# Kernel optimization log

Measured on AMD Instinct MI355X. Metric: run time of the kernel, lower is better.

The kernel has to match this reference:

```python
import jax, jax.numpy as jnp
import numpy as np

NHEAD = 8

def setup_inputs() -> dict:
    key = jax.random.key(0)
    k1, k2, k3, k4 = jax.random.split(key, 4)
    B, N, I, KQ, V = 2, 4096, 512, 512, 512
    x = jax.random.normal(k1, (B, N, I), dtype=jnp.float32)
    # store weights as [in, out] so projection is x @ W (same math as torch Linear with W.T)
    Wk = jax.random.normal(k2, (I, KQ), dtype=jnp.float32) * (1.0 / np.sqrt(I))
    Wq = jax.random.normal(k3, (I, KQ), dtype=jnp.float32) * (1.0 / np.sqrt(I))
    Wv = jax.random.normal(k4, (I, V), dtype=jnp.float32) * (1.0 / np.sqrt(I))
    return {"x": x, "Wk": Wk, "Wq": Wq, "Wv": Wv}

def reference(x, Wk, Wq, Wv):
    B, N, _ = x.shape
    H = NHEAD
    k = (x @ Wk).reshape(B, N, H, -1)   # [B,N,H,dk]
    q = (x @ Wq).reshape(B, N, H, -1)   # [B,N,H,dk]
    v = (x @ Wv).reshape(B, N, H, -1)   # [B,N,H,dv]
    dk = k.shape[-1]
    # scores[b,n,m,h] = k[b,n,h,:] . q[b,m,h,:] / sqrt(dk)
    scores = jnp.einsum('bnhd,bmhd->bnmh', k, q) / jnp.sqrt(jnp.asarray(dk, x.dtype))
    attn = jax.nn.softmax(scores, axis=-2)  # softmax over m (dim -2), matching torch code
    out = jnp.einsum('bnmh,bmhd->bnhd', attn, v)
    return out.reshape(B, N, -1)
```

## Files before the change

kernel.cpp:

```cpp
#include <hip/hip_runtime.h>
#include <hip/hip_bf16.h>

typedef __bf16 bf16_t;
typedef bf16_t bf16x8 __attribute__((ext_vector_type(8)));
typedef bf16_t bf16x4 __attribute__((ext_vector_type(4)));
typedef float f32x4 __attribute__((ext_vector_type(4)));

#define MFMA16(a, b, c) __builtin_amdgcn_mfma_f32_16x16x32_bf16(a, b, c, 0, 0, 0)

typedef __attribute__((address_space(3))) unsigned int lds_u32_t;
typedef __attribute__((address_space(1))) const unsigned int glb_u32_t;

__device__ __forceinline__ void gload16(const void* g, void* l) {
    __builtin_amdgcn_global_load_lds((glb_u32_t*)g, (lds_u32_t*)l, 16, 0, 0);
}

__device__ __forceinline__ bf16x8 lds8(const bf16_t* base, int row, int cb) {
    return *reinterpret_cast<const bf16x8*>(
        reinterpret_cast<const char*>(base) + row * 128 + (cb ^ ((row & 7) << 4)));
}

__global__ __launch_bounds__(256) void prep_kernel(
    const float* __restrict__ X,
    const float* __restrict__ Wq, const float* __restrict__ Wk,
    const float* __restrict__ Wv,
    bf16_t* __restrict__ Xb, bf16_t* __restrict__ Wt)
{
    __shared__ float T[64][65];
    if (blockIdx.x < 2048) {
        const size_t i = ((size_t)blockIdx.x * 256 + threadIdx.x) * 8;
        const float4 v0 = *reinterpret_cast<const float4*>(&X[i]);
        const float4 v1 = *reinterpret_cast<const float4*>(&X[i + 4]);
        bf16x8 o;
        o[0] = (bf16_t)v0.x; o[1] = (bf16_t)v0.y; o[2] = (bf16_t)v0.z; o[3] = (bf16_t)v0.w;
        o[4] = (bf16_t)v1.x; o[5] = (bf16_t)v1.y; o[6] = (bf16_t)v1.z; o[7] = (bf16_t)v1.w;
        *reinterpret_cast<bf16x8*>(&Xb[i]) = o;
        return;
    }
    const int idx = (int)blockIdx.x - 2048;
    const int mat = idx >> 6;
    const int rem = idx & 63;
    const int k0 = (rem >> 3) * 64, n0 = (rem & 7) * 64;
    const float* W = (mat == 0) ? Wq : (mat == 1 ? Wk : Wv);
    const int r = threadIdx.x >> 4, c4 = (threadIdx.x & 15) * 4;

    for (int rep = 0; rep < 4; ++rep) {
        const int row = r + rep * 16;
        const float4 v = *reinterpret_cast<const float4*>(&W[(size_t)(k0 + row) * 512 + n0 + c4]);
        T[row][c4 + 0] = v.x; T[row][c4 + 1] = v.y;
        T[row][c4 + 2] = v.z; T[row][c4 + 3] = v.w;
    }
    __syncthreads();
    const float scl = (mat == 1) ? 0.1803368801111204f : 1.0f;
    for (int rep = 0; rep < 4; ++rep) {
        const int nrow = r + rep * 16;
        bf16x4 o;
        for (int e = 0; e < 4; ++e) o[e] = (bf16_t)(T[c4 + e][nrow] * scl);
        *reinterpret_cast<bf16x4*>(&Wt[(size_t)mat * 262144 + (size_t)(n0 + nrow) * 512 + k0 + c4]) = o;
    }
}

__global__ __launch_bounds__(256, 2) void proj_bf16(
    const bf16_t* __restrict__ Xb, const bf16_t* __restrict__ Wt,
    bf16_t* __restrict__ Qb, bf16_t* __restrict__ Kb, bf16_t* __restrict__ Vt)
{
    __shared__ __align__(16) char smemP[65536];
    bf16_t* Ab0 = (bf16_t*)smemP;
    bf16_t* Bb0 = (bf16_t*)(smemP + 32768);

    const int tid = threadIdx.x;
    const int w = tid >> 6, l = tid & 63, g = l >> 4, lr = l & 15;
    const int m0 = blockIdx.x * 128;
    const int mat = blockIdx.y >> 2;
    const int n0 = (blockIdx.y & 3) * 128;
    const bf16_t* Wm = Wt + (size_t)mat * 262144;
    const int wm = (w >> 1) * 64, wn = (w & 1) * 64;

#define STAGE_P(buf, k0v)                                                   \
    do {                                                                    \
        for (int t = 0; t < 4; ++t) {                                       \
            const int rb = w * 32 + t * 8;                                  \
            const int row = rb + (l >> 3);                                  \
            const int cb = ((l & 7) << 4) ^ ((row & 7) << 4);               \
            gload16(&Xb[(size_t)(m0 + row) * 512 + (k0v) + (cb >> 1)],      \
                    Ab0 + (buf) * 8192 + rb * 64);                          \
            gload16(&Wm[(size_t)(n0 + row) * 512 + (k0v) + (cb >> 1)],      \
                    Bb0 + (buf) * 8192 + rb * 64);                          \
        }                                                                   \
    } while (0)

    f32x4 acc[4][4];
    const f32x4 z4 = {0.f, 0.f, 0.f, 0.f};
#pragma unroll
    for (int i = 0; i < 4; ++i)
#pragma unroll
        for (int j = 0; j < 4; ++j) acc[i][j] = z4;

    STAGE_P(0, 0);
    __syncthreads();

    for (int kk = 0; kk < 8; ++kk) {
        const int cur = kk & 1;
        if (kk + 1 < 8) STAGE_P(cur ^ 1, (kk + 1) * 64);

        bf16x8 a[4][2], bq[4][2];
#pragma unroll
        for (int fa = 0; fa < 4; ++fa)
#pragma unroll
            for (int dh = 0; dh < 2; ++dh) {
                a[fa][dh]  = lds8(Ab0 + cur * 8192, wm + fa * 16 + lr, dh * 64 + g * 16);
                bq[fa][dh] = lds8(Bb0 + cur * 8192, wn + fa * 16 + lr, dh * 64 + g * 16);
            }
        __builtin_amdgcn_s_setprio(1);
#pragma unroll
        for (int fa = 0; fa < 4; ++fa)
#pragma unroll
            for (int fb = 0; fb < 4; ++fb) {
                acc[fa][fb] = MFMA16(a[fa][0], bq[fb][0], acc[fa][fb]);
                acc[fa][fb] = MFMA16(a[fa][1], bq[fb][1], acc[fa][fb]);
            }
        __builtin_amdgcn_s_setprio(0);
        __syncthreads();
    }
#undef STAGE_P

    if (mat <= 1) {
        bf16_t* C = (mat == 0) ? Qb : Kb;
#pragma unroll
        for (int fa = 0; fa < 4; ++fa)
#pragma unroll
            for (int fb = 0; fb < 4; ++fb) {
                bf16x4 v4;
#pragma unroll
                for (int j = 0; j < 4; ++j) v4[j] = (bf16_t)acc[fa][fb][j];
#pragma unroll
                for (int j = 0; j < 4; ++j) {
                    const int m = m0 + wm + fa * 16 + g * 4 + j;
                    const int n = n0 + wn + fb * 16 + lr;
                    C[(size_t)m * 512 + n] = v4[j];
                }
            }
        return;
    }

    bf16_t* vt_lds = (bf16_t*)smemP;
#pragma unroll
    for (int fa = 0; fa < 4; ++fa)
#pragma unroll
        for (int fb = 0; fb < 4; ++fb) {
            const int ml = wm + fa * 16 + g * 4;
            const int loc = ml & 63;
            const int p = (loc & 32) | (((loc >> 2) & 3) << 3) |
                          (((loc >> 4) & 1) << 2) | (loc & 3);
            const int col = ((ml >> 6) << 6) + p;
            const int nl = wn + fb * 16 + lr;
            bf16x4 v4;
#pragma unroll
            for (int j = 0; j < 4; ++j) v4[j] = (bf16_t)acc[fa][fb][j];
            *reinterpret_cast<bf16x4*>(&vt_lds[nl * 132 + col]) = v4;
        }
    __syncthreads();

    const int hh0 = n0 >> 6;
    const int b_ = m0 >> 12;
    const int mt0 = (m0 & 4095) >> 6;
#pragma unroll
    for (int pass = 0; pass < 8; ++pass) {
        const int unit = pass * 32 + w * 8 + (l >> 3);
        const int row = unit & 127;
        const int mt_half = unit >> 7;
        const int d = row & 63, hh = hh0 + (row >> 6);
        const int bh_ = b_ * 8 + hh;
        const int mt = mt0 + mt_half;
        const bf16x8 v8 = *reinterpret_cast<const bf16x8*>(
            &vt_lds[row * 132 + mt_half * 64 + (l & 7) * 8]);
        *reinterpret_cast<bf16x8*>(
            &Vt[(size_t)bh_ * 262144 + (size_t)mt * 4096 + d * 64 + (l & 7) * 8]) = v8;
    }
}

__global__ __launch_bounds__(256) void proj_kernel(
    const float* __restrict__ X,
    const float* __restrict__ Wq, const float* __restrict__ Wk,
    const float* __restrict__ Wv,
    bf16_t* __restrict__ Qb, bf16_t* __restrict__ Kb, bf16_t* __restrict__ Vt)
{
    __shared__ bf16_t Ax[128][40];
    __shared__ bf16_t Wtl[64][40];

    const int mode = blockIdx.z;
    const float* W = (mode == 0) ? Wq : (mode == 1 ? Wk : Wv);
    bf16_t* C = (mode == 0) ? Qb : (mode == 1 ? Kb : Vt);

    const int tid = threadIdx.x;
    const int w = tid >> 6, l = tid & 63, g = l >> 4, lr = l & 15;
    const int m0 = blockIdx.x * 128, n0 = blockIdx.y * 64;

    f32x4 acc[2][4];
    const f32x4 z4 = {0.f, 0.f, 0.f, 0.f};
    for (int i = 0; i < 2; ++i)
        for (int j = 0; j < 4; ++j) acc[i][j] = z4;

    for (int k0 = 0; k0 < 512; k0 += 32) {
        {
            const int c4 = (tid & 7) * 4;
            for (int r = 0; r < 4; ++r) {
                const int row = (tid >> 3) + r * 32;
                const float4 v = *reinterpret_cast<const float4*>(
                    &X[(size_t)(m0 + row) * 512 + k0 + c4]);
                bf16x4 o;
                o[0] = (bf16_t)v.x; o[1] = (bf16_t)v.y;
                o[2] = (bf16_t)v.z; o[3] = (bf16_t)v.w;
                *reinterpret_cast<bf16x4*>(&Ax[row][c4]) = o;
            }
        }
        {
            const int c4 = (tid & 15) * 4;
            for (int r = 0; r < 2; ++r) {
                const int krow = (tid >> 4) + r * 16;
                const float4 v = *reinterpret_cast<const float4*>(
                    &W[(size_t)(k0 + krow) * 512 + n0 + c4]);
                Wtl[c4 + 0][krow] = (bf16_t)v.x;
                Wtl[c4 + 1][krow] = (bf16_t)v.y;
                Wtl[c4 + 2][krow] = (bf16_t)v.z;
                Wtl[c4 + 3][krow] = (bf16_t)v.w;
            }
        }
        __syncthreads();

        bf16x8 a[2], bq[4];
        for (int fr = 0; fr < 2; ++fr)
            a[fr] = *reinterpret_cast<const bf16x8*>(&Ax[w * 32 + fr * 16 + lr][g * 8]);
        for (int fn = 0; fn < 4; ++fn)
            bq[fn] = *reinterpret_cast<const bf16x8*>(&Wtl[fn * 16 + lr][g * 8]);
        for (int fr = 0; fr < 2; ++fr)
            for (int fn = 0; fn < 4; ++fn)
                acc[fr][fn] = MFMA16(a[fr], bq[fn], acc[fr][fn]);
        __syncthreads();
    }

    const float SCL = 0.125f * 1.44269504088896f;
    for (int fr = 0; fr < 2; ++fr)
        for (int fn = 0; fn < 4; ++fn)
            for (int j = 0; j < 4; ++j) {
                const int m = m0 + w * 32 + fr * 16 + g * 4 + j;
                const int n = n0 + fn * 16 + lr;
                float vf = acc[fr][fn][j];
                if (mode == 1) vf *= SCL;
                const bf16_t val = (bf16_t)vf;
                if (mode <= 1) {
                    C[(size_t)m * 512 + n] = val;
                } else {
                    const int b_ = m >> 12, mm = m & 4095;
                    const int hh = n >> 6, d = n & 63;
                    const int loc = mm & 63;
                    const int p = (loc & 32) | (((loc >> 2) & 3) << 3) |
                                  (((loc >> 4) & 1) << 2) | (loc & 3);
                    C[(size_t)(b_ * 8 + hh) * 262144 +
                      (size_t)(mm >> 6) * 4096 + d * 64 + p] = val;
                }
            }
}

__global__ __launch_bounds__(512, 2) void attn_kernel(
    const bf16_t* __restrict__ Kb, const bf16_t* __restrict__ Qb,
    const bf16_t* __restrict__ Vt, float* __restrict__ Out)
{
    __shared__ __align__(16) char smem[65536];

    const int tid = threadIdx.x;
    const int w = tid >> 6, l = tid & 63, g = l >> 4, lr = l & 15;
    const int mh = w >> 2;
    const int u = w & 3;

    const int id = ((int)blockIdx.x & 7) * 64 + ((int)blockIdx.x >> 3);
    const int bh = id >> 5, nb = id & 31;
    const int b = bh >> 3, hd = bh & 7;
    const int n0 = nb * 128;
    const int t0 = mh * 32;

    bf16x8 ak[2][2];
#pragma unroll
    for (int fr = 0; fr < 2; ++fr)
#pragma unroll
        for (int dh = 0; dh < 2; ++dh)
            ak[fr][dh] = *reinterpret_cast<const bf16x8*>(
                &Kb[(size_t)(b * 4096 + n0 + u * 32 + fr * 16 + lr) * 512 +
                    hd * 64 + dh * 32 + g * 8]);

    bf16x8 ones;
#pragma unroll
    for (int i = 0; i < 8; ++i) ones[i] = (bf16_t)1.0f;

#define STAGE(buf, m0v)                                                              \
    do {                                                                             \
        char* qls = smem + mh * 32768 + (buf) * 16384;                               \
        char* vls = qls + 8192;                                                      \
        for (int t = 0; t < 2; ++t) {                                                \
            const int row = u * 16 + t * 8 + (l >> 3);                               \
            const int cb = ((l & 7) << 4) ^ ((row & 7) << 4);                        \
            gload16(&Qb[(size_t)(b * 4096 + (m0v) + row) * 512 + hd * 64 + (cb >> 1)],\
                    qls + (u * 16 + t * 8) * 128);                                   \
            gload16(&Vt[(size_t)bh * 262144 + (size_t)((m0v) >> 6) * 4096 +          \
                        row * 64 + (cb >> 1)],                                       \
                    vls + (u * 16 + t * 8) * 128);                                   \
        }                                                                            \
    } while (0)

    f32x4 acc[2][4];
    f32x4 dacc[2];
    const f32x4 z4 = {0.f, 0.f, 0.f, 0.f};
#pragma unroll
    for (int fr = 0; fr < 2; ++fr) {
        dacc[fr] = z4;
#pragma unroll
        for (int j = 0; j < 4; ++j) acc[fr][j] = z4;
    }

    auto compute_tile = [&](int buf) {
        const bf16_t* qb = (const bf16_t*)(smem + mh * 32768 + buf * 16384);
        const bf16_t* vb = (const bf16_t*)(smem + mh * 32768 + buf * 16384 + 8192);

        f32x4 s[4][2];
#pragma unroll
        for (int m16 = 0; m16 < 4; ++m16)
#pragma unroll
            for (int fr = 0; fr < 2; ++fr) s[m16][fr] = z4;

        __builtin_amdgcn_s_setprio(1);
#pragma unroll
        for (int m16 = 0; m16 < 4; ++m16) {
            const int r = m16 * 16 + lr;
            const bf16x8 a0 = lds8(qb, r, g * 16);
            const bf16x8 a1 = lds8(qb, r, 64 + g * 16);
            s[m16][0] = MFMA16(a0, ak[0][0], s[m16][0]);
            s[m16][0] = MFMA16(a1, ak[0][1], s[m16][0]);
            s[m16][1] = MFMA16(a0, ak[1][0], s[m16][1]);
            s[m16][1] = MFMA16(a1, ak[1][1], s[m16][1]);
        }
        __builtin_amdgcn_s_setprio(0);

        bf16x8 pa[2][2];
#pragma unroll
        for (int fr = 0; fr < 2; ++fr)
#pragma unroll
            for (int c = 0; c < 2; ++c)
#pragma unroll
                for (int e = 0; e < 8; ++e)
                    pa[fr][c][e] = (bf16_t)__builtin_amdgcn_exp2f(
                        s[c * 2 + (e >> 2)][fr][e & 3]);

        __builtin_amdgcn_s_setprio(1);
        dacc[0] = MFMA16(pa[0][0], ones, dacc[0]);
        dacc[0] = MFMA16(pa[0][1], ones, dacc[0]);
        dacc[1] = MFMA16(pa[1][0], ones, dacc[1]);
        dacc[1] = MFMA16(pa[1][1], ones, dacc[1]);
#pragma unroll
        for (int fd = 0; fd < 4; ++fd) {
            const bf16x8 vb0 = lds8(vb, fd * 16 + lr, g * 16);
            const bf16x8 vb1 = lds8(vb, fd * 16 + lr, 64 + g * 16);
            acc[0][fd] = MFMA16(pa[0][0], vb0, acc[0][fd]);
            acc[0][fd] = MFMA16(pa[0][1], vb1, acc[0][fd]);
            acc[1][fd] = MFMA16(pa[1][0], vb0, acc[1][fd]);
            acc[1][fd] = MFMA16(pa[1][1], vb1, acc[1][fd]);
        }
        __builtin_amdgcn_s_setprio(0);
    };

    STAGE(0, t0 * 64);
    __syncthreads();

    for (int it = 0; it < 32; ++it) {
        if (it + 1 < 32) STAGE((it + 1) & 1, (t0 + it + 1) * 64);
        compute_tile(it & 1);
        __syncthreads();
    }

    float* comb = (float*)smem;
    float* cden = (float*)(smem + 33280);

    if (mh == 1) {
#pragma unroll
        for (int fr = 0; fr < 2; ++fr)
#pragma unroll
            for (int fd = 0; fd < 4; ++fd)
#pragma unroll
                for (int j = 0; j < 4; ++j)
                    comb[(u * 32 + fr * 16 + g * 4 + j) * 65 + fd * 16 + lr] =
                        acc[fr][fd][j];
        if (lr == 0) {
#pragma unroll
            for (int fr = 0; fr < 2; ++fr)
#pragma unroll
                for (int j = 0; j < 4; ++j)
                    cden[u * 32 + fr * 16 + g * 4 + j] = dacc[fr][j];
        }
    }
    __syncthreads();
    if (mh == 0) {
        float linv[2][4];
#pragma unroll
        for (int fr = 0; fr < 2; ++fr)
#pragma unroll
            for (int j = 0; j < 4; ++j) {
                const int nl = u * 32 + fr * 16 + g * 4 + j;
                linv[fr][j] = 1.0f / (dacc[fr][j] + cden[nl]);
            }
#pragma unroll
        for (int fr = 0; fr < 2; ++fr)
#pragma unroll
            for (int fd = 0; fd < 4; ++fd)
#pragma unroll
                for (int j = 0; j < 4; ++j) {
                    const int nl = u * 32 + fr * 16 + g * 4 + j;
                    const int d = fd * 16 + lr;
                    Out[((size_t)(b * 4096 + n0 + nl)) * 512 + hd * 64 + d] =
                        (acc[fr][fd][j] + comb[nl * 65 + d]) * linv[fr][j];
                }
    }
#undef STAGE
}

extern "C" void kernel_launch(void* const* d_in, const int* in_sizes, int n_in,
                              void* d_out, int out_size, void* d_ws, size_t ws_size,
                              hipStream_t stream)
{
    const float* x  = (const float*)d_in[0];
    const float* Wk = (const float*)d_in[1];
    const float* Wq = (const float*)d_in[2];
    const float* Wv = (const float*)d_in[3];
    float* out = (float*)d_out;

    char* ws = (char*)d_ws;
    bf16_t* Kb = (bf16_t*)ws;
    bf16_t* Qb = Kb + (size_t)4194304;
    bf16_t* Vt = Qb + (size_t)4194304;
    bf16_t* Xb = (bf16_t*)(ws + 25165824);
    bf16_t* Wt = Xb + (size_t)4194304;

    const size_t NEED_PRE = 35127296;
    const bool has_pre = ws_size >= NEED_PRE;

    if (has_pre) {
        hipLaunchKernelGGL(prep_kernel, dim3(2240), dim3(256), 0, stream,
                           x, Wq, Wk, Wv, Xb, Wt);
        hipLaunchKernelGGL(proj_bf16, dim3(64, 12), dim3(256), 0, stream,
                           Xb, Wt, Qb, Kb, Vt);
    } else {
        hipLaunchKernelGGL(proj_kernel, dim3(64, 8, 3), dim3(256), 0, stream,
                           x, Wq, Wk, Wv, Qb, Kb, Vt);
    }

    hipLaunchKernelGGL(attn_kernel, dim3(512), dim3(512), 0, stream,
                       Kb, Qb, Vt, out);
}
```

Before: 90.39 us.

## Split score tile in halves to overlap exp with PV MFMA; scalar row sums

The per-tile score computation is split into two halves. The exp/convert of the first half can then overlap with the second half's QK MFMAs and the first half's PV MFMAs. The softmax denominator is no longer computed with MFMAs against a ones vector. Each lane accumulates an fp32 scalar sum, reduced with cross-lane shuffles after the loop. This removes four MFMAs per tile and shrinks the live score registers, at the cost of extra VALU adds and a denominator summed from unrounded fp32 values instead of bf16-rounded ones.

```diff
diff --git a/kernel.cpp b/kernel.cpp
--- a/kernel.cpp
+++ b/kernel.cpp
@@ -130,14 +130,11 @@
         for (int fa = 0; fa < 4; ++fa)
 #pragma unroll
             for (int fb = 0; fb < 4; ++fb) {
-                bf16x4 v4;
-#pragma unroll
-                for (int j = 0; j < 4; ++j) v4[j] = (bf16_t)acc[fa][fb][j];
 #pragma unroll
                 for (int j = 0; j < 4; ++j) {
                     const int m = m0 + wm + fa * 16 + g * 4 + j;
                     const int n = n0 + wn + fb * 16 + lr;
-                    C[(size_t)m * 512 + n] = v4[j];
+                    C[(size_t)m * 512 + n] = (bf16_t)acc[fa][fb][j];
                 }
             }
         return;
@@ -288,10 +285,6 @@
                 &Kb[(size_t)(b * 4096 + n0 + u * 32 + fr * 16 + lr) * 512 +
                     hd * 64 + dh * 32 + g * 8]);
 
-    bf16x8 ones;
-#pragma unroll
-    for (int i = 0; i < 8; ++i) ones[i] = (bf16_t)1.0f;
-
 #define STAGE(buf, m0v)                                                              \
     do {                                                                             \
         char* qls = smem + mh * 32768 + (buf) * 16384;                               \
@@ -308,11 +301,11 @@
     } while (0)
 
     f32x4 acc[2][4];
-    f32x4 dacc[2];
+    float dl[2];
     const f32x4 z4 = {0.f, 0.f, 0.f, 0.f};
 #pragma unroll
     for (int fr = 0; fr < 2; ++fr) {
-        dacc[fr] = z4;
+        dl[fr] = 0.f;
 #pragma unroll
         for (int j = 0; j < 4; ++j) acc[fr][j] = z4;
     }
@@ -320,49 +313,76 @@
     auto compute_tile = [&](int buf) {
         const bf16_t* qb = (const bf16_t*)(smem + mh * 32768 + buf * 16384);
         const bf16_t* vb = (const bf16_t*)(smem + mh * 32768 + buf * 16384 + 8192);
-
-        f32x4 s[4][2];
-#pragma unroll
-        for (int m16 = 0; m16 < 4; ++m16)
-#pragma unroll
-            for (int fr = 0; fr < 2; ++fr) s[m16][fr] = z4;
+        bf16x8 pa[2][2];
+
+        {
+            f32x4 s[2][2];
+#pragma unroll
+            for (int mm = 0; mm < 2; ++mm)
+#pragma unroll
+                for (int fr = 0; fr < 2; ++fr) s[mm][fr] = z4;
+            __builtin_amdgcn_s_setprio(1);
+#pragma unroll
+            for (int mm = 0; mm < 2; ++mm) {
+                const int r = mm * 16 + lr;
+                const bf16x8 a0 = lds8(qb, r, g * 16);
+                const bf16x8 a1 = lds8(qb, r, 64 + g * 16);
+                s[mm][0] = MFMA16(a0, ak[0][0], s[mm][0]);
+                s[mm][0] = MFMA16(a1, ak[0][1], s[mm][0]);
+                s[mm][1] = MFMA16(a0, ak[1][0], s[mm][1]);
+                s[mm][1] = MFMA16(a1, ak[1][1], s[mm][1]);
+            }
+            __builtin_amdgcn_s_setprio(0);
+#pragma unroll
+            for (int fr = 0; fr < 2; ++fr)
+#pragma unroll
+                for (int e = 0; e < 8; ++e) {
+                    const float p = __builtin_amdgcn_exp2f(s[e >> 2][fr][e & 3]);
+                    dl[fr] += p;
+                    pa[fr][0][e] = (bf16_t)p;
+                }
+        }
+
+        {
+            f32x4 s[2][2];
+#pragma unroll
+            for (int mm = 0; mm < 2; ++mm)
+#pragma unroll
+                for (int fr = 0; fr < 2; ++fr) s[mm][fr] = z4;
+            __builtin_amdgcn_s_setprio(1);
+#pragma unroll
+            for (int mm = 0; mm < 2; ++mm) {
+                const int r = (2 + mm) * 16 + lr;
+                const bf16x8 a0 = lds8(qb, r, g * 16);
+                const bf16x8 a1 = lds8(qb, r, 64 + g * 16);
+                s[mm][0] = MFMA16(a0, ak[0][0], s[mm][0]);
+                s[mm][0] = MFMA16(a1, ak[0][1], s[mm][0]);
+                s[mm][1] = MFMA16(a0, ak[1][0], s[mm][1]);
+                s[mm][1] = MFMA16(a1, ak[1][1], s[mm][1]);
+            }
+#pragma unroll
+            for (int fd = 0; fd < 4; ++fd) {
+                const bf16x8 v0 = lds8(vb, fd * 16 + lr, g * 16);
+                acc[0][fd] = MFMA16(pa[0][0], v0, acc[0][fd]);
+                acc[1][fd] = MFMA16(pa[1][0], v0, acc[1][fd]);
+            }
+            __builtin_amdgcn_s_setprio(0);
+#pragma unroll
+            for (int fr = 0; fr < 2; ++fr)
+#pragma unroll
+                for (int e = 0; e < 8; ++e) {
+                    const float p = __builtin_amdgcn_exp2f(s[e >> 2][fr][e & 3]);
+                    dl[fr] += p;
+                    pa[fr][1][e] = (bf16_t)p;
+                }
+        }
 
         __builtin_amdgcn_s_setprio(1);
 #pragma unroll
-        for (int m16 = 0; m16 < 4; ++m16) {
-            const int r = m16 * 16 + lr;
-            const bf16x8 a0 = lds8(qb, r, g * 16);
-            const bf16x8 a1 = lds8(qb, r, 64 + g * 16);
-            s[m16][0] = MFMA16(a0, ak[0][0], s[m16][0]);
-            s[m16][0] = MFMA16(a1, ak[0][1], s[m16][0]);
-            s[m16][1] = MFMA16(a0, ak[1][0], s[m16][1]);
-            s[m16][1] = MFMA16(a1, ak[1][1], s[m16][1]);
-        }
-        __builtin_amdgcn_s_setprio(0);
-
-        bf16x8 pa[2][2];
-#pragma unroll
-        for (int fr = 0; fr < 2; ++fr)
-#pragma unroll
-            for (int c = 0; c < 2; ++c)
-#pragma unroll
-                for (int e = 0; e < 8; ++e)
-                    pa[fr][c][e] = (bf16_t)__builtin_amdgcn_exp2f(
-                        s[c * 2 + (e >> 2)][fr][e & 3]);
-
-        __builtin_amdgcn_s_setprio(1);
-        dacc[0] = MFMA16(pa[0][0], ones, dacc[0]);
-        dacc[0] = MFMA16(pa[0][1], ones, dacc[0]);
-        dacc[1] = MFMA16(pa[1][0], ones, dacc[1]);
-        dacc[1] = MFMA16(pa[1][1], ones, dacc[1]);
-#pragma unroll
         for (int fd = 0; fd < 4; ++fd) {
-            const bf16x8 vb0 = lds8(vb, fd * 16 + lr, g * 16);
-            const bf16x8 vb1 = lds8(vb, fd * 16 + lr, 64 + g * 16);
-            acc[0][fd] = MFMA16(pa[0][0], vb0, acc[0][fd]);
-            acc[0][fd] = MFMA16(pa[0][1], vb1, acc[0][fd]);
-            acc[1][fd] = MFMA16(pa[1][0], vb0, acc[1][fd]);
-            acc[1][fd] = MFMA16(pa[1][1], vb1, acc[1][fd]);
+            const bf16x8 v1 = lds8(vb, fd * 16 + lr, 64 + g * 16);
+            acc[0][fd] = MFMA16(pa[0][1], v1, acc[0][fd]);
+            acc[1][fd] = MFMA16(pa[1][1], v1, acc[1][fd]);
         }
         __builtin_amdgcn_s_setprio(0);
     };
@@ -376,6 +396,17 @@
         __syncthreads();
     }
 
+    float denr[2][4];
+#pragma unroll
+    for (int fr = 0; fr < 2; ++fr) {
+        float d = dl[fr];
+        d += __shfl_xor(d, 16);
+        d += __shfl_xor(d, 32);
+#pragma unroll
+        for (int j = 0; j < 4; ++j)
+            denr[fr][j] = __shfl(d, g * 4 + j);
+    }
+
     float* comb = (float*)smem;
     float* cden = (float*)(smem + 33280);
 
@@ -393,7 +424,7 @@
             for (int fr = 0; fr < 2; ++fr)
 #pragma unroll
                 for (int j = 0; j < 4; ++j)
-                    cden[u * 32 + fr * 16 + g * 4 + j] = dacc[fr][j];
+                    cden[u * 32 + fr * 16 + g * 4 + j] = denr[fr][j];
         }
     }
     __syncthreads();
@@ -404,7 +435,7 @@
 #pragma unroll
             for (int j = 0; j < 4; ++j) {
                 const int nl = u * 32 + fr * 16 + g * 4 + j;
-                linv[fr][j] = 1.0f / (dacc[fr][j] + cden[nl]);
+                linv[fr][j] = 1.0f / (denr[fr][j] + cden[nl]);
             }
 #pragma unroll
         for (int fr = 0; fr < 2; ++fr)
```

After: 99.47 us. 1.1x slower.
